# Kernel tuning notes

Measured on AMD Instinct MI355X. Metric: run time of the kernel, lower is better.

Reference implementation:

```python
import jax, jax.numpy as jnp
import numpy as np

B, L = 8192, 16
H, DK, DV = 8, 32, 32
DM, BN, V = 256, 128, 50000
NEG = -1e32  # mask_fill_value from masked_softmax(memory_efficient=True)


def layer_norm(x, g, b, eps=1e-5):
    m = jnp.mean(x, axis=-1, keepdims=True)
    var = jnp.mean((x - m) ** 2, axis=-1, keepdims=True)
    return (x - m) / jnp.sqrt(var + eps) * g + b


def setup_inputs() -> dict:
    key = jax.random.key(0)
    ks = iter(jax.random.split(key, 40))

    def n(shape, s):
        return jax.random.normal(next(ks), shape, jnp.float32) * s

    s_qk = float(np.sqrt(2.0 / (DM + DK)))
    s_v = float(np.sqrt(2.0 / (DM + DV)))
    d = {"x": jax.random.randint(next(ks), (B, L), 0, V)}
    d.update({
        "node_emb": n((V, BN), 1.0),
        "ln1_g": jnp.ones(BN), "ln1_b": jnp.zeros(BN),
        "ln2_g": jnp.ones(BN), "ln2_b": jnp.zeros(BN),
        "ln3_g": jnp.ones(BN), "ln3_b": jnp.zeros(BN),
        "Wq": n((H * DK, BN), s_qk), "Wk": n((H * DK, BN), s_qk), "Wv": n((H * DV, BN), s_v),
        "Wfc1": n((DM, H * DV), 0.05),
        "p1_w1": n((DM, DM), 0.05), "p1_b1": jnp.zeros(DM),
        "p1_w2": n((DM, DM), 0.05), "p1_b2": jnp.zeros(DM),
        "p1_lng": jnp.ones(DM), "p1_lnb": jnp.zeros(DM),
        "p2_w1": n((DM, BN), 0.05), "p2_b1": jnp.zeros(DM),
        "p2_w2": n((DM, DM), 0.05), "p2_b2": jnp.zeros(DM),
        "lnc1_g": jnp.ones(DM), "lnc1_b": jnp.zeros(DM),
        "lnc2_g": jnp.ones(DM), "lnc2_b": jnp.zeros(DM),
        "Wcls": n((1, DM), 0.05), "bcls": jnp.zeros(1),
    })
    return d


def reference(x, node_emb, ln1_g, ln1_b, ln2_g, ln2_b, ln3_g, ln3_b,
              Wq, Wk, Wv, Wfc1,
              p1_w1, p1_b1, p1_w2, p1_b2, p1_lng, p1_lnb,
              p2_w1, p2_b1, p2_w2, p2_b2,
              lnc1_g, lnc1_b, lnc2_g, lnc2_b, Wcls, bcls):
    b, l = x.shape
    emb = node_emb[x]                                  # [B,L,BN]
    npm = (x != 0).astype(jnp.float32)[..., None]      # non-pad mask [B,L,1]
    # MultiHeadAttention (eval mode, dropout off). Note: the slf_attn_mask
    # positional arg is overwritten inside forward by the ones-minus-eye
    # diag mask, and mask=None, so only diagonal self-exclusion applies.
    q = (layer_norm(emb, ln1_g, ln1_b) @ Wq.T).reshape(b, l, H, DK)
    k = (layer_norm(emb, ln2_g, ln2_b) @ Wk.T).reshape(b, l, H, DK)
    v = (layer_norm(emb, ln3_g, ln3_b) @ Wv.T).reshape(b, l, H, DV)
    scores = jnp.einsum('blhd,bmhd->bhlm', q, k) / jnp.sqrt(jnp.float32(DK))
    scores = jnp.where(jnp.eye(l, dtype=bool), NEG, scores)
    attn = jax.nn.softmax(scores, axis=-1)
    ctx = jnp.einsum('bhlm,bmhd->blhd', attn, v).reshape(b, l, H * DV)
    # fc1 + pff_n1 (residual + layer_norm since dims equal)
    dyn_in = (ctx @ Wfc1.T) * npm
    h1 = jnp.tanh(dyn_in @ p1_w1.T + p1_b1)
    dynamic = layer_norm(h1 @ p1_w2.T + p1_b2 + dyn_in, p1_lng, p1_lnb) * npm
    # pff_n2 on original (static) embedding; bottle_neck != d_model so no
    # residual / layer_norm. (The MHA fc2 static output is discarded by
    # EncoderLayer, so it is not computed here.)
    sta_in = emb * npm
    static = (jnp.tanh(sta_in @ p2_w1.T + p2_b1) @ p2_w2.T + p2_b2) * npm
    # Classifier head: diag_mask_flag=='True' -> (dynamic - static)**2
    dyn = layer_norm(dynamic, lnc1_g, lnc1_b)
    sta = layer_norm(static, lnc2_g, lnc2_b)
    probs = jax.nn.sigmoid((dyn - sta) ** 2 @ Wcls.T + bcls)  # [B,L,1]
    return jnp.sum(probs * npm, axis=1) / jnp.sum(npm, axis=1)  # [B,1]
```

## Files before the change

kernel.cpp:

```cpp
#include <hip/hip_runtime.h>
#include <math.h>

typedef unsigned short u16;
typedef _Float16 f16;
typedef f16 f16x4 __attribute__((ext_vector_type(4)));
typedef f16 f16x8v __attribute__((ext_vector_type(8)));
typedef float f32x4 __attribute__((ext_vector_type(4)));


__device__ __forceinline__ float tanh_f(float x) {
  float e = __expf(2.f * x);
  return 1.f - 2.f / (e + 1.f);
}

__device__ __forceinline__ void stage_chunk(const u16* __restrict__ wall, u16* wbuf,
                                            int si, int ds, int wid, int lane) {
  const u16* src = wall + (size_t)si * 8192;
  u16* dst = wbuf + ds * 8192;
#pragma unroll
  for (int j = 0; j < 2; ++j) {
    __builtin_amdgcn_global_load_lds(
        (const __attribute__((address_space(1))) void*)(src + j * 4096 + wid * 512 + lane * 8),
        (__attribute__((address_space(3))) void*)(dst + j * 4096 + wid * 512), 16, 0, 0);
  }
}

__device__ __forceinline__ const u16* pipe_acq(const u16* __restrict__ wall, u16* wbuf,
                                               int c, int wid, int lane) {
  int nx = c + 2;
  if (nx >= 48) nx -= 48;
  stage_chunk(wall, wbuf, nx, (c + 2) & 3, wid, lane);
  asm volatile("s_waitcnt vmcnt(4)" ::: "memory");
  __builtin_amdgcn_sched_barrier(0);
  __builtin_amdgcn_s_barrier();
  __builtin_amdgcn_sched_barrier(0);
  return wbuf + (c & 3) * 8192;
}

template <int PT, bool SW>
__device__ __forceinline__ f32x4 tile_mm32(const u16* buf, int lt, const f16x8v* bfr,
                                           int lane) {
  f32x4 a = {};
#pragma unroll
  for (int p = 0; p < PT; ++p) {
    f16x8v w = *(const f16x8v*)(buf + (lt * PT + p) * 512 + (size_t)lane * 8);
    if constexpr (!SW)
      a = __builtin_amdgcn_mfma_f32_16x16x32_f16(w, bfr[p], a, 0, 0, 0);
    else
      a = __builtin_amdgcn_mfma_f32_16x16x32_f16(bfr[p], w, a, 0, 0, 0);
  }
  return a;
}

__global__ __launch_bounds__(512) void fused_kernel(
    const int* __restrict__ x, const float* __restrict__ node_emb,
    const u16* __restrict__ wall, const float* __restrict__ aux,
    const float* __restrict__ p1_b1, const float* __restrict__ p1_b2,
    const float* __restrict__ p1_lng, const float* __restrict__ p1_lnb,
    const float* __restrict__ p2_b1, const float* __restrict__ p2_b2,
    const float* __restrict__ lnc1_g, const float* __restrict__ lnc1_b,
    const float* __restrict__ lnc2_g, const float* __restrict__ lnc2_b,
    const float* __restrict__ Wcls, const float* __restrict__ bcls,
    float* __restrict__ out) {
  __shared__ __align__(16) u16 wbuf[32768];
  const int lane = threadIdx.x & 63;
  const int wid = threadIdx.x >> 6;
  const int sr = lane & 15, g = lane >> 4;
  const int elem = blockIdx.x * 8 + wid;

  const int xi = x[elem * 16 + sr];
  const float npm = (xi != 0) ? 1.f : 0.f;

  stage_chunk(wall, wbuf, 0, 0, wid, lane);
  stage_chunk(wall, wbuf, 1, 1, wid, lane);

  f16x8v ebf8[4];
  float mu, rs;
  {
    const float4* erow = (const float4*)(node_emb + (size_t)xi * 128 + g * 4);
    float su = 0.f, sq = 0.f;
#pragma unroll
    for (int t = 0; t < 8; ++t) {
      float4 v = erow[t * 4];
      su += v.x + v.y + v.z + v.w;
      sq += v.x * v.x + v.y * v.y + v.z * v.z + v.w * v.w;
      const int hb = (t & 1) * 4;
      ebf8[t >> 1][hb + 0] = (f16)v.x;
      ebf8[t >> 1][hb + 1] = (f16)v.y;
      ebf8[t >> 1][hb + 2] = (f16)v.z;
      ebf8[t >> 1][hb + 3] = (f16)v.w;
    }
    su += __shfl_xor(su, 16); su += __shfl_xor(su, 32);
    sq += __shfl_xor(sq, 16); sq += __shfl_xor(sq, 32);
    mu = su * (1.f / 128.f);
    rs = rsqrtf(sq * (1.f / 128.f) - mu * mu + 1e-5f);
  }

  int c = 0;

  f16x8v qf8[8];
#pragma unroll
  for (int cc = 0; cc < 4; ++cc) {
    const u16* buf = pipe_acq(wall, wbuf, c, wid, lane);
#pragma unroll
    for (int lt = 0; lt < 4; ++lt) {
      f32x4 a = tile_mm32<4, false>(buf, lt, ebf8, lane);
      const int T = cc * 4 + lt;
      float4 G4 = *(const float4*)(aux + T * 16 + g * 4);
      float4 B4 = *(const float4*)(aux + 256 + T * 16 + g * 4);
      const int hb = (T & 1) * 4;
#pragma unroll
      for (int i = 0; i < 4; ++i)
        qf8[T >> 1][hb + i] =
            (f16)(rs * (a[i] - mu * ((const float*)&G4)[i]) + ((const float*)&B4)[i]);
    }
    ++c;
  }

  f16x4 pb[8];
#pragma unroll
  for (int cc = 0; cc < 4; ++cc) {
    const u16* buf = pipe_acq(wall, wbuf, c, wid, lane);
#pragma unroll
    for (int hh = 0; hh < 2; ++hh) {
      f16x8v kt8;
#pragma unroll
      for (int sub = 0; sub < 2; ++sub) {
        f32x4 a = tile_mm32<4, false>(buf, hh * 2 + sub, ebf8, lane);
        const int T = cc * 4 + hh * 2 + sub;
        float4 G4 = *(const float4*)(aux + 512 + T * 16 + g * 4);
        float4 B4 = *(const float4*)(aux + 512 + 256 + T * 16 + g * 4);
#pragma unroll
        for (int i = 0; i < 4; ++i)
          kt8[sub * 4 + i] =
              (f16)(rs * (a[i] - mu * ((const float*)&G4)[i]) + ((const float*)&B4)[i]);
      }
      const int h = cc * 2 + hh;
      f32x4 s4 = {};
      s4 = __builtin_amdgcn_mfma_f32_16x16x32_f16(kt8, qf8[h], s4, 0, 0, 0);
      float e4[4], mx = -3.0e38f;
#pragma unroll
      for (int i = 0; i < 4; ++i) {
        float v = s4[i] * 0.17677669529663687f;
        if ((g * 4 + i) == sr) v = -3.0e38f;
        e4[i] = v;
        mx = fmaxf(mx, v);
      }
      mx = fmaxf(mx, __shfl_xor(mx, 16));
      mx = fmaxf(mx, __shfl_xor(mx, 32));
      float sm = 0.f;
#pragma unroll
      for (int i = 0; i < 4; ++i) {
        e4[i] = ((g * 4 + i) == sr) ? 0.f : __expf(e4[i] - mx);
        sm += e4[i];
      }
      sm += __shfl_xor(sm, 16);
      sm += __shfl_xor(sm, 32);
      float inv = 1.f / sm;
#pragma unroll
      for (int i = 0; i < 4; ++i) pb[h][i] = (f16)(e4[i] * inv);
    }
    ++c;
  }

  f16x8v cf8[8];
  {
    float mur[4], rsr[4];
#pragma unroll
    for (int i = 0; i < 4; ++i) {
      mur[i] = __shfl(mu, g * 4 + i);
      rsr[i] = __shfl(rs, g * 4 + i);
    }
#pragma unroll
    for (int cc = 0; cc < 4; ++cc) {
      const u16* buf = pipe_acq(wall, wbuf, c, wid, lane);
#pragma unroll
      for (int lt = 0; lt < 4; ++lt) {
        f32x4 a = tile_mm32<4, true>(buf, lt, ebf8, lane);
        const int T = cc * 4 + lt;
        float Gv = aux[1024 + T * 16 + sr];
        float Bv = aux[1024 + 256 + T * 16 + sr];
        f16x4 vt;
#pragma unroll
        for (int i = 0; i < 4; ++i) vt[i] = (f16)(rsr[i] * (a[i] - mur[i] * Gv) + Bv);
        f32x4 cacc = {};
        cacc = __builtin_amdgcn_mfma_f32_16x16x16f16(vt, pb[T >> 1], cacc, 0, 0, 0);
        const int hb = (T & 1) * 4;
#pragma unroll
        for (int i = 0; i < 4; ++i) cf8[T >> 1][hb + i] = (f16)cacc[i];
      }
      ++c;
    }
  }

  f16x8v dinf8[8];
#pragma unroll
  for (int cc = 0; cc < 8; ++cc) {
    const u16* buf = pipe_acq(wall, wbuf, c, wid, lane);
#pragma unroll
    for (int lt = 0; lt < 2; ++lt) {
      f32x4 a = tile_mm32<8, false>(buf, lt, cf8, lane);
      const int T = cc * 2 + lt;
      const int hb = (T & 1) * 4;
#pragma unroll
      for (int i = 0; i < 4; ++i) dinf8[T >> 1][hb + i] = (f16)(a[i] * npm);
    }
    ++c;
  }

  f16x8v h1f8[8];
#pragma unroll
  for (int cc = 0; cc < 8; ++cc) {
    const u16* buf = pipe_acq(wall, wbuf, c, wid, lane);
#pragma unroll
    for (int lt = 0; lt < 2; ++lt) {
      f32x4 a = tile_mm32<8, false>(buf, lt, dinf8, lane);
      const int T = cc * 2 + lt;
      float4 b = *(const float4*)(p1_b1 + T * 16 + g * 4);
      const int hb = (T & 1) * 4;
#pragma unroll
      for (int i = 0; i < 4; ++i)
        h1f8[T >> 1][hb + i] = (f16)tanh_f(a[i] + ((const float*)&b)[i]);
    }
    ++c;
  }

  f16x4 d1f[16];
  float s1 = 0.f, s2 = 0.f;
#pragma unroll
  for (int cc = 0; cc < 8; ++cc) {
    const u16* buf = pipe_acq(wall, wbuf, c, wid, lane);
#pragma unroll
    for (int lt = 0; lt < 2; ++lt) {
      f32x4 a = tile_mm32<8, false>(buf, lt, h1f8, lane);
      const int T = cc * 2 + lt;
      float4 b = *(const float4*)(p1_b2 + T * 16 + g * 4);
      const int hb = (T & 1) * 4;
#pragma unroll
      for (int i = 0; i < 4; ++i) {
        float v = a[i] + ((const float*)&b)[i] + (float)dinf8[T >> 1][hb + i];
        s1 += v;
        s2 += v * v;
        d1f[T][i] = (f16)v;
      }
    }
    ++c;
  }
  s1 += __shfl_xor(s1, 16); s1 += __shfl_xor(s1, 32);
  s2 += __shfl_xor(s2, 16); s2 += __shfl_xor(s2, 32);
  const float muA = s1 * (1.f / 256.f);
  const float rsA = rsqrtf(s2 * (1.f / 256.f) - muA * muA + 1e-5f);

  f16x8v s1f8[8];
#pragma unroll
  for (int cc = 0; cc < 4; ++cc) {
    const u16* buf = pipe_acq(wall, wbuf, c, wid, lane);
#pragma unroll
    for (int lt = 0; lt < 4; ++lt) {
      f32x4 a = tile_mm32<4, false>(buf, lt, ebf8, lane);
      const int T = cc * 4 + lt;
      float4 b = *(const float4*)(p2_b1 + T * 16 + g * 4);
      const int hb = (T & 1) * 4;
#pragma unroll
      for (int i = 0; i < 4; ++i)
        s1f8[T >> 1][hb + i] = (f16)tanh_f(npm * a[i] + ((const float*)&b)[i]);
    }
    ++c;
  }

  float M_puu = 0.f, M_qvv = 0.f, M_pquv = 0.f;
  float M_pug = 0.f, M_ppu = 0.f, M_pqu = 0.f;
  float M_qvg = 0.f, M_pqv = 0.f, M_qqv = 0.f;
  float t1 = 0.f, t2 = 0.f, v1 = 0.f, v2 = 0.f;
#pragma unroll
  for (int cc = 0; cc < 8; ++cc) {
    const u16* buf = pipe_acq(wall, wbuf, c, wid, lane);
#pragma unroll
    for (int lt = 0; lt < 2; ++lt) {
      f32x4 av = tile_mm32<8, false>(buf, lt, s1f8, lane);
      const int T = cc * 2 + lt;
      float4 b2 = *(const float4*)(p2_b2 + T * 16 + g * 4);
      float4 lg = *(const float4*)(p1_lng + T * 16 + g * 4);
      float4 lb = *(const float4*)(p1_lnb + T * 16 + g * 4);
      float4 wc = *(const float4*)(Wcls + T * 16 + g * 4);
      float4 pg4 = *(const float4*)(lnc1_g + T * 16 + g * 4);
      float4 qg4 = *(const float4*)(lnc2_g + T * 16 + g * 4);
      float4 eb4 = *(const float4*)(lnc1_b + T * 16 + g * 4);
      float4 fb4 = *(const float4*)(lnc2_b + T * 16 + g * 4);
#pragma unroll
      for (int i = 0; i < 4; ++i) {
        float v = (av[i] + ((const float*)&b2)[i]) * npm;
        float u = (((float)d1f[T][i] - muA) * rsA * ((const float*)&lg)[i] +
                   ((const float*)&lb)[i]) * npm;
        t1 += u; t2 += u * u; v1 += v; v2 += v * v;
        float gc = ((const float*)&eb4)[i] - ((const float*)&fb4)[i];
        float pu = ((const float*)&pg4)[i] * u;
        float qv = ((const float*)&qg4)[i] * v;
        float wpu = ((const float*)&wc)[i] * pu;
        float wqv = ((const float*)&wc)[i] * qv;
        M_puu = fmaf(wpu, pu, M_puu);
        M_qvv = fmaf(wqv, qv, M_qvv);
        M_pquv = fmaf(wpu, qv, M_pquv);
        M_pug = fmaf(wpu, gc, M_pug);
        M_ppu = fmaf(wpu, ((const float*)&pg4)[i], M_ppu);
        M_pqu = fmaf(wpu, ((const float*)&qg4)[i], M_pqu);
        M_qvg = fmaf(wqv, gc, M_qvg);
        M_pqv = fmaf(wqv, ((const float*)&pg4)[i], M_pqv);
        M_qqv = fmaf(wqv, ((const float*)&qg4)[i], M_qqv);
      }
    }
    ++c;
  }
  asm volatile("s_waitcnt vmcnt(0)" ::: "memory");

#define RED2(z) z += __shfl_xor(z, 16); z += __shfl_xor(z, 32);
  RED2(t1) RED2(t2) RED2(v1) RED2(v2)
  RED2(M_puu) RED2(M_qvv) RED2(M_pquv)
  RED2(M_pug) RED2(M_ppu) RED2(M_pqu)
  RED2(M_qvg) RED2(M_pqv) RED2(M_qqv)
#undef RED2
  const float muD = t1 * (1.f / 256.f);
  const float aD = rsqrtf(t2 * (1.f / 256.f) - muD * muD + 1e-5f);
  const float muS = v1 * (1.f / 256.f);
  const float bS = rsqrtf(v2 * (1.f / 256.f) - muS * muS + 1e-5f);
  const float* s6 = aux + 1536;
  float logit = aD * aD * M_puu + bS * bS * M_qvv - 2.f * aD * bS * M_pquv
      + 2.f * aD * (M_pug - aD * muD * M_ppu + bS * muS * M_pqu)
      - 2.f * bS * (M_qvg - aD * muD * M_pqv + bS * muS * M_qqv)
      + s6[0] - 2.f * aD * muD * s6[1] + 2.f * bS * muS * s6[2]
      + aD * aD * muD * muD * s6[3] + bS * bS * muS * muS * s6[4]
      - 2.f * aD * bS * muD * muS * s6[5]
      + bcls[0];
  float prob = npm / (1.f + __expf(-logit));
  float ns = npm;
#pragma unroll
  for (int o = 1; o < 16; o <<= 1) {
    prob += __shfl_xor(prob, o);
    ns += __shfl_xor(ns, o);
  }
  if (lane == 0) out[elem] = prob / ns;
}

__global__ void prep_all(const float* __restrict__ Wq, const float* __restrict__ Wk,
                         const float* __restrict__ Wv, const float* __restrict__ Wfc1,
                         const float* __restrict__ p1w1, const float* __restrict__ p1w2,
                         const float* __restrict__ p2w1, const float* __restrict__ p2w2,
                         const float* __restrict__ g1, const float* __restrict__ b1,
                         const float* __restrict__ g2, const float* __restrict__ b2,
                         const float* __restrict__ g3, const float* __restrict__ b3,
                         const float* __restrict__ c1g, const float* __restrict__ c1b,
                         const float* __restrict__ c2g, const float* __restrict__ c2b,
                         const float* __restrict__ Wc,
                         u16* __restrict__ ws, float* __restrict__ aux) {
  int bx = blockIdx.x, t = threadIdx.x;
  if (bx == 1539) {
    if (t == 0) {
      float mgg = 0.f, mpg = 0.f, mqg = 0.f, mpp = 0.f, mqq = 0.f, mpq = 0.f;
      for (int cx = 0; cx < 256; ++cx) {
        float W = Wc[cx], p = c1g[cx], q = c2g[cx], gg = c1b[cx] - c2b[cx];
        mgg += W * gg * gg; mpg += W * p * gg; mqg += W * q * gg;
        mpp += W * p * p; mqq += W * q * q; mpq += W * p * q;
      }
      aux[1536] = mgg; aux[1537] = mpg; aux[1538] = mqg;
      aux[1539] = mpp; aux[1540] = mqq; aux[1541] = mpq;
    }
    return;
  }
  if (bx >= 1536) {
    int m = bx - 1536;
    const float* W = (m == 0) ? Wq : (m == 1) ? Wk : Wv;
    const float* gg = (m == 0) ? g1 : (m == 1) ? g2 : g3;
    const float* bb = (m == 0) ? b1 : (m == 1) ? b2 : b3;
    float G = 0.f, Bv = 0.f;
    for (int k = 0; k < 128; ++k) {
      float w = W[t * 128 + k];
      G += w * gg[k];
      Bv += w * bb[k];
    }
    aux[m * 512 + t] = G;
    aux[m * 512 + 256 + t] = Bv;
    return;
  }
  const float* src;
  u16* dst;
  const float* sc = nullptr;
  int base, K;
  if (bx < 128) {
    src = Wq; dst = ws; sc = g1; base = bx; K = 128;
  } else if (bx < 256) {
    src = Wk; dst = ws + 32768; sc = g2; base = bx - 128; K = 128;
  } else if (bx < 384) {
    src = Wv; dst = ws + 65536; sc = g3; base = bx - 256; K = 128;
  } else if (bx < 640) {
    src = Wfc1; dst = ws + 98304; base = bx - 384; K = 256;
  } else if (bx < 896) {
    src = p1w1; dst = ws + 163840; base = bx - 640; K = 256;
  } else if (bx < 1152) {
    src = p1w2; dst = ws + 229376; base = bx - 896; K = 256;
  } else if (bx < 1280) {
    src = p2w1; dst = ws + 294912; base = bx - 1152; K = 128;
  } else {
    src = p2w2; dst = ws + 327680; base = bx - 1280; K = 256;
  }
  int i = base * 256 + t;
  int n, k;
  if (K == 128) {
    n = i >> 7; k = i & 127;
  } else {
    n = i >> 8; k = i & 255;
  }
  float v = src[i];
  if (sc) v *= sc[k];
  int blk = (n >> 4) * (K >> 4) + (k >> 4);
  int l = (((k >> 2) & 3) << 4) + (n & 15);
  int di = ((blk >> 1) << 9) + (l << 3) + ((blk & 1) << 2) + (k & 3);
  dst[di] = __builtin_bit_cast(u16, (f16)v);
}

extern "C" void kernel_launch(void* const* d_in, const int* in_sizes, int n_in,
                              void* d_out, int out_size, void* d_ws, size_t ws_size,
                              hipStream_t stream) {
  const int* x = (const int*)d_in[0];
  const float* node_emb = (const float*)d_in[1];
  const float* ln1_g = (const float*)d_in[2];
  const float* ln1_b = (const float*)d_in[3];
  const float* ln2_g = (const float*)d_in[4];
  const float* ln2_b = (const float*)d_in[5];
  const float* ln3_g = (const float*)d_in[6];
  const float* ln3_b = (const float*)d_in[7];
  const float* Wq = (const float*)d_in[8];
  const float* Wk = (const float*)d_in[9];
  const float* Wv = (const float*)d_in[10];
  const float* Wfc1 = (const float*)d_in[11];
  const float* p1_w1 = (const float*)d_in[12];
  const float* p1_b1 = (const float*)d_in[13];
  const float* p1_w2 = (const float*)d_in[14];
  const float* p1_b2 = (const float*)d_in[15];
  const float* p1_lng = (const float*)d_in[16];
  const float* p1_lnb = (const float*)d_in[17];
  const float* p2_w1 = (const float*)d_in[18];
  const float* p2_b1 = (const float*)d_in[19];
  const float* p2_w2 = (const float*)d_in[20];
  const float* p2_b2 = (const float*)d_in[21];
  const float* lnc1_g = (const float*)d_in[22];
  const float* lnc1_b = (const float*)d_in[23];
  const float* lnc2_g = (const float*)d_in[24];
  const float* lnc2_b = (const float*)d_in[25];
  const float* Wcls = (const float*)d_in[26];
  const float* bcls = (const float*)d_in[27];

  u16* ws = (u16*)d_ws;
  float* aux = (float*)(ws + 393216);

  prep_all<<<1540, 256, 0, stream>>>(Wq, Wk, Wv, Wfc1, p1_w1, p1_w2, p2_w1, p2_w2, ln1_g, ln1_b,
                                     ln2_g, ln2_b, ln3_g, ln3_b, lnc1_g, lnc1_b, lnc2_g, lnc2_b,
                                     Wcls, ws, aux);

  const int B = in_sizes[0] / 16;
  fused_kernel<<<B / 8, 512, 0, stream>>>(
      x, node_emb, ws, aux, p1_b1, p1_b2, p1_lng, p1_lnb, p2_b1, p2_b2, lnc1_g, lnc1_b, lnc2_g,
      lnc2_b, Wcls, bcls, (float*)d_out);
}
```

Before: 212.9 us.

## Shrink blocks to 4 waves with smaller chunks and 3-deep 5-buffer weight pipeline

Each block now has 256 threads covering 4 batch elements instead of 512 threads and 8, so twice as many blocks are launched. Weight chunks are halved to 8 KB, staged three ahead into a 5-slot LDS ring (40 KB rather than 64 KB), and every stage loop is re-tiled so it consumes 96 chunks instead of 48. The aim is lower LDS use per block, more resident blocks and deeper prefetch that hides global-to-LDS latency. In exchange there are twice as many block barriers per element and each loaded weight chunk is reused by only 4 waves, which raises weight traffic.

```diff
diff --git a/kernel.cpp b/kernel.cpp
--- a/kernel.cpp
+++ b/kernel.cpp
@@ -15,26 +15,27 @@
 
 __device__ __forceinline__ void stage_chunk(const u16* __restrict__ wall, u16* wbuf,
                                             int si, int ds, int wid, int lane) {
-  const u16* src = wall + (size_t)si * 8192;
-  u16* dst = wbuf + ds * 8192;
+  const u16* src = wall + (size_t)si * 4096;
+  u16* dst = wbuf + ds * 4096;
 #pragma unroll
   for (int j = 0; j < 2; ++j) {
+    int seg = wid * 2 + j;
     __builtin_amdgcn_global_load_lds(
-        (const __attribute__((address_space(1))) void*)(src + j * 4096 + wid * 512 + lane * 8),
-        (__attribute__((address_space(3))) void*)(dst + j * 4096 + wid * 512), 16, 0, 0);
+        (const __attribute__((address_space(1))) void*)(src + seg * 512 + lane * 8),
+        (__attribute__((address_space(3))) void*)(dst + seg * 512), 16, 0, 0);
   }
 }
 
 __device__ __forceinline__ const u16* pipe_acq(const u16* __restrict__ wall, u16* wbuf,
                                                int c, int wid, int lane) {
-  int nx = c + 2;
-  if (nx >= 48) nx -= 48;
-  stage_chunk(wall, wbuf, nx, (c + 2) & 3, wid, lane);
-  asm volatile("s_waitcnt vmcnt(4)" ::: "memory");
+  int nx = c + 3;
+  if (nx >= 96) nx -= 96;
+  stage_chunk(wall, wbuf, nx, (c + 3) % 5, wid, lane);
+  asm volatile("s_waitcnt vmcnt(6)" ::: "memory");
   __builtin_amdgcn_sched_barrier(0);
   __builtin_amdgcn_s_barrier();
   __builtin_amdgcn_sched_barrier(0);
-  return wbuf + (c & 3) * 8192;
+  return wbuf + (c % 5) * 4096;
 }
 
 template <int PT, bool SW>
@@ -52,7 +53,7 @@
   return a;
 }
 
-__global__ __launch_bounds__(512) void fused_kernel(
+__global__ __launch_bounds__(256) void fused_kernel(
     const int* __restrict__ x, const float* __restrict__ node_emb,
     const u16* __restrict__ wall, const float* __restrict__ aux,
     const float* __restrict__ p1_b1, const float* __restrict__ p1_b2,
@@ -62,17 +63,18 @@
     const float* __restrict__ lnc2_g, const float* __restrict__ lnc2_b,
     const float* __restrict__ Wcls, const float* __restrict__ bcls,
     float* __restrict__ out) {
-  __shared__ __align__(16) u16 wbuf[32768];
+  __shared__ __align__(16) u16 wbuf[20480];
   const int lane = threadIdx.x & 63;
   const int wid = threadIdx.x >> 6;
   const int sr = lane & 15, g = lane >> 4;
-  const int elem = blockIdx.x * 8 + wid;
+  const int elem = blockIdx.x * 4 + wid;
 
   const int xi = x[elem * 16 + sr];
   const float npm = (xi != 0) ? 1.f : 0.f;
 
   stage_chunk(wall, wbuf, 0, 0, wid, lane);
   stage_chunk(wall, wbuf, 1, 1, wid, lane);
+  stage_chunk(wall, wbuf, 2, 2, wid, lane);
 
   f16x8v ebf8[4];
   float mu, rs;
@@ -100,12 +102,12 @@
 
   f16x8v qf8[8];
 #pragma unroll
-  for (int cc = 0; cc < 4; ++cc) {
-    const u16* buf = pipe_acq(wall, wbuf, c, wid, lane);
-#pragma unroll
-    for (int lt = 0; lt < 4; ++lt) {
+  for (int cc = 0; cc < 8; ++cc) {
+    const u16* buf = pipe_acq(wall, wbuf, c, wid, lane);
+#pragma unroll
+    for (int lt = 0; lt < 2; ++lt) {
       f32x4 a = tile_mm32<4, false>(buf, lt, ebf8, lane);
-      const int T = cc * 4 + lt;
+      const int T = cc * 2 + lt;
       float4 G4 = *(const float4*)(aux + T * 16 + g * 4);
       float4 B4 = *(const float4*)(aux + 256 + T * 16 + g * 4);
       const int hb = (T & 1) * 4;
@@ -119,47 +121,43 @@
 
   f16x4 pb[8];
 #pragma unroll
-  for (int cc = 0; cc < 4; ++cc) {
-    const u16* buf = pipe_acq(wall, wbuf, c, wid, lane);
-#pragma unroll
-    for (int hh = 0; hh < 2; ++hh) {
-      f16x8v kt8;
-#pragma unroll
-      for (int sub = 0; sub < 2; ++sub) {
-        f32x4 a = tile_mm32<4, false>(buf, hh * 2 + sub, ebf8, lane);
-        const int T = cc * 4 + hh * 2 + sub;
-        float4 G4 = *(const float4*)(aux + 512 + T * 16 + g * 4);
-        float4 B4 = *(const float4*)(aux + 512 + 256 + T * 16 + g * 4);
-#pragma unroll
-        for (int i = 0; i < 4; ++i)
-          kt8[sub * 4 + i] =
-              (f16)(rs * (a[i] - mu * ((const float*)&G4)[i]) + ((const float*)&B4)[i]);
-      }
-      const int h = cc * 2 + hh;
-      f32x4 s4 = {};
-      s4 = __builtin_amdgcn_mfma_f32_16x16x32_f16(kt8, qf8[h], s4, 0, 0, 0);
-      float e4[4], mx = -3.0e38f;
-#pragma unroll
-      for (int i = 0; i < 4; ++i) {
-        float v = s4[i] * 0.17677669529663687f;
-        if ((g * 4 + i) == sr) v = -3.0e38f;
-        e4[i] = v;
-        mx = fmaxf(mx, v);
-      }
-      mx = fmaxf(mx, __shfl_xor(mx, 16));
-      mx = fmaxf(mx, __shfl_xor(mx, 32));
-      float sm = 0.f;
-#pragma unroll
-      for (int i = 0; i < 4; ++i) {
-        e4[i] = ((g * 4 + i) == sr) ? 0.f : __expf(e4[i] - mx);
-        sm += e4[i];
-      }
-      sm += __shfl_xor(sm, 16);
-      sm += __shfl_xor(sm, 32);
-      float inv = 1.f / sm;
-#pragma unroll
-      for (int i = 0; i < 4; ++i) pb[h][i] = (f16)(e4[i] * inv);
-    }
+  for (int cc = 0; cc < 8; ++cc) {
+    const u16* buf = pipe_acq(wall, wbuf, c, wid, lane);
+    f16x8v kt8;
+#pragma unroll
+    for (int sub = 0; sub < 2; ++sub) {
+      f32x4 a = tile_mm32<4, false>(buf, sub, ebf8, lane);
+      const int T = cc * 2 + sub;
+      float4 G4 = *(const float4*)(aux + 512 + T * 16 + g * 4);
+      float4 B4 = *(const float4*)(aux + 512 + 256 + T * 16 + g * 4);
+#pragma unroll
+      for (int i = 0; i < 4; ++i)
+        kt8[sub * 4 + i] =
+            (f16)(rs * (a[i] - mu * ((const float*)&G4)[i]) + ((const float*)&B4)[i]);
+    }
+    f32x4 s4 = {};
+    s4 = __builtin_amdgcn_mfma_f32_16x16x32_f16(kt8, qf8[cc], s4, 0, 0, 0);
+    float e4[4], mx = -3.0e38f;
+#pragma unroll
+    for (int i = 0; i < 4; ++i) {
+      float v = s4[i] * 0.17677669529663687f;
+      if ((g * 4 + i) == sr) v = -3.0e38f;
+      e4[i] = v;
+      mx = fmaxf(mx, v);
+    }
+    mx = fmaxf(mx, __shfl_xor(mx, 16));
+    mx = fmaxf(mx, __shfl_xor(mx, 32));
+    float sm = 0.f;
+#pragma unroll
+    for (int i = 0; i < 4; ++i) {
+      e4[i] = ((g * 4 + i) == sr) ? 0.f : __expf(e4[i] - mx);
+      sm += e4[i];
+    }
+    sm += __shfl_xor(sm, 16);
+    sm += __shfl_xor(sm, 32);
+    float inv = 1.f / sm;
+#pragma unroll
+    for (int i = 0; i < 4; ++i) pb[cc][i] = (f16)(e4[i] * inv);
     ++c;
   }
 
@@ -172,12 +170,12 @@
       rsr[i] = __shfl(rs, g * 4 + i);
     }
 #pragma unroll
-    for (int cc = 0; cc < 4; ++cc) {
+    for (int cc = 0; cc < 8; ++cc) {
       const u16* buf = pipe_acq(wall, wbuf, c, wid, lane);
 #pragma unroll
-      for (int lt = 0; lt < 4; ++lt) {
+      for (int lt = 0; lt < 2; ++lt) {
         f32x4 a = tile_mm32<4, true>(buf, lt, ebf8, lane);
-        const int T = cc * 4 + lt;
+        const int T = cc * 2 + lt;
         float Gv = aux[1024 + T * 16 + sr];
         float Bv = aux[1024 + 256 + T * 16 + sr];
         f16x4 vt;
@@ -195,54 +193,42 @@
 
   f16x8v dinf8[8];
 #pragma unroll
-  for (int cc = 0; cc < 8; ++cc) {
-    const u16* buf = pipe_acq(wall, wbuf, c, wid, lane);
-#pragma unroll
-    for (int lt = 0; lt < 2; ++lt) {
-      f32x4 a = tile_mm32<8, false>(buf, lt, cf8, lane);
-      const int T = cc * 2 + lt;
-      const int hb = (T & 1) * 4;
-#pragma unroll
-      for (int i = 0; i < 4; ++i) dinf8[T >> 1][hb + i] = (f16)(a[i] * npm);
-    }
+  for (int T = 0; T < 16; ++T) {
+    const u16* buf = pipe_acq(wall, wbuf, c, wid, lane);
+    f32x4 a = tile_mm32<8, false>(buf, 0, cf8, lane);
+    const int hb = (T & 1) * 4;
+#pragma unroll
+    for (int i = 0; i < 4; ++i) dinf8[T >> 1][hb + i] = (f16)(a[i] * npm);
     ++c;
   }
 
   f16x8v h1f8[8];
 #pragma unroll
-  for (int cc = 0; cc < 8; ++cc) {
-    const u16* buf = pipe_acq(wall, wbuf, c, wid, lane);
-#pragma unroll
-    for (int lt = 0; lt < 2; ++lt) {
-      f32x4 a = tile_mm32<8, false>(buf, lt, dinf8, lane);
-      const int T = cc * 2 + lt;
-      float4 b = *(const float4*)(p1_b1 + T * 16 + g * 4);
-      const int hb = (T & 1) * 4;
-#pragma unroll
-      for (int i = 0; i < 4; ++i)
-        h1f8[T >> 1][hb + i] = (f16)tanh_f(a[i] + ((const float*)&b)[i]);
-    }
+  for (int T = 0; T < 16; ++T) {
+    const u16* buf = pipe_acq(wall, wbuf, c, wid, lane);
+    f32x4 a = tile_mm32<8, false>(buf, 0, dinf8, lane);
+    float4 b = *(const float4*)(p1_b1 + T * 16 + g * 4);
+    const int hb = (T & 1) * 4;
+#pragma unroll
+    for (int i = 0; i < 4; ++i)
+      h1f8[T >> 1][hb + i] = (f16)tanh_f(a[i] + ((const float*)&b)[i]);
     ++c;
   }
 
   f16x4 d1f[16];
   float s1 = 0.f, s2 = 0.f;
 #pragma unroll
-  for (int cc = 0; cc < 8; ++cc) {
-    const u16* buf = pipe_acq(wall, wbuf, c, wid, lane);
-#pragma unroll
-    for (int lt = 0; lt < 2; ++lt) {
-      f32x4 a = tile_mm32<8, false>(buf, lt, h1f8, lane);
-      const int T = cc * 2 + lt;
-      float4 b = *(const float4*)(p1_b2 + T * 16 + g * 4);
-      const int hb = (T & 1) * 4;
-#pragma unroll
-      for (int i = 0; i < 4; ++i) {
-        float v = a[i] + ((const float*)&b)[i] + (float)dinf8[T >> 1][hb + i];
-        s1 += v;
-        s2 += v * v;
-        d1f[T][i] = (f16)v;
-      }
+  for (int T = 0; T < 16; ++T) {
+    const u16* buf = pipe_acq(wall, wbuf, c, wid, lane);
+    f32x4 a = tile_mm32<8, false>(buf, 0, h1f8, lane);
+    float4 b = *(const float4*)(p1_b2 + T * 16 + g * 4);
+    const int hb = (T & 1) * 4;
+#pragma unroll
+    for (int i = 0; i < 4; ++i) {
+      float v = a[i] + ((const float*)&b)[i] + (float)dinf8[T >> 1][hb + i];
+      s1 += v;
+      s2 += v * v;
+      d1f[T][i] = (f16)v;
     }
     ++c;
   }
@@ -253,12 +239,12 @@
 
   f16x8v s1f8[8];
 #pragma unroll
-  for (int cc = 0; cc < 4; ++cc) {
-    const u16* buf = pipe_acq(wall, wbuf, c, wid, lane);
-#pragma unroll
-    for (int lt = 0; lt < 4; ++lt) {
+  for (int cc = 0; cc < 8; ++cc) {
+    const u16* buf = pipe_acq(wall, wbuf, c, wid, lane);
+#pragma unroll
+    for (int lt = 0; lt < 2; ++lt) {
       f32x4 a = tile_mm32<4, false>(buf, lt, ebf8, lane);
-      const int T = cc * 4 + lt;
+      const int T = cc * 2 + lt;
       float4 b = *(const float4*)(p2_b1 + T * 16 + g * 4);
       const int hb = (T & 1) * 4;
 #pragma unroll
@@ -273,41 +259,37 @@
   float M_qvg = 0.f, M_pqv = 0.f, M_qqv = 0.f;
   float t1 = 0.f, t2 = 0.f, v1 = 0.f, v2 = 0.f;
 #pragma unroll
-  for (int cc = 0; cc < 8; ++cc) {
-    const u16* buf = pipe_acq(wall, wbuf, c, wid, lane);
-#pragma unroll
-    for (int lt = 0; lt < 2; ++lt) {
-      f32x4 av = tile_mm32<8, false>(buf, lt, s1f8, lane);
-      const int T = cc * 2 + lt;
-      float4 b2 = *(const float4*)(p2_b2 + T * 16 + g * 4);
-      float4 lg = *(const float4*)(p1_lng + T * 16 + g * 4);
-      float4 lb = *(const float4*)(p1_lnb + T * 16 + g * 4);
-      float4 wc = *(const float4*)(Wcls + T * 16 + g * 4);
-      float4 pg4 = *(const float4*)(lnc1_g + T * 16 + g * 4);
-      float4 qg4 = *(const float4*)(lnc2_g + T * 16 + g * 4);
-      float4 eb4 = *(const float4*)(lnc1_b + T * 16 + g * 4);
-      float4 fb4 = *(const float4*)(lnc2_b + T * 16 + g * 4);
-#pragma unroll
-      for (int i = 0; i < 4; ++i) {
-        float v = (av[i] + ((const float*)&b2)[i]) * npm;
-        float u = (((float)d1f[T][i] - muA) * rsA * ((const float*)&lg)[i] +
-                   ((const float*)&lb)[i]) * npm;
-        t1 += u; t2 += u * u; v1 += v; v2 += v * v;
-        float gc = ((const float*)&eb4)[i] - ((const float*)&fb4)[i];
-        float pu = ((const float*)&pg4)[i] * u;
-        float qv = ((const float*)&qg4)[i] * v;
-        float wpu = ((const float*)&wc)[i] * pu;
-        float wqv = ((const float*)&wc)[i] * qv;
-        M_puu = fmaf(wpu, pu, M_puu);
-        M_qvv = fmaf(wqv, qv, M_qvv);
-        M_pquv = fmaf(wpu, qv, M_pquv);
-        M_pug = fmaf(wpu, gc, M_pug);
-        M_ppu = fmaf(wpu, ((const float*)&pg4)[i], M_ppu);
-        M_pqu = fmaf(wpu, ((const float*)&qg4)[i], M_pqu);
-        M_qvg = fmaf(wqv, gc, M_qvg);
-        M_pqv = fmaf(wqv, ((const float*)&pg4)[i], M_pqv);
-        M_qqv = fmaf(wqv, ((const float*)&qg4)[i], M_qqv);
-      }
+  for (int T = 0; T < 16; ++T) {
+    const u16* buf = pipe_acq(wall, wbuf, c, wid, lane);
+    f32x4 av = tile_mm32<8, false>(buf, 0, s1f8, lane);
+    float4 b2 = *(const float4*)(p2_b2 + T * 16 + g * 4);
+    float4 lg = *(const float4*)(p1_lng + T * 16 + g * 4);
+    float4 lb = *(const float4*)(p1_lnb + T * 16 + g * 4);
+    float4 wc = *(const float4*)(Wcls + T * 16 + g * 4);
+    float4 pg4 = *(const float4*)(lnc1_g + T * 16 + g * 4);
+    float4 qg4 = *(const float4*)(lnc2_g + T * 16 + g * 4);
+    float4 eb4 = *(const float4*)(lnc1_b + T * 16 + g * 4);
+    float4 fb4 = *(const float4*)(lnc2_b + T * 16 + g * 4);
+#pragma unroll
+    for (int i = 0; i < 4; ++i) {
+      float v = (av[i] + ((const float*)&b2)[i]) * npm;
+      float u = (((float)d1f[T][i] - muA) * rsA * ((const float*)&lg)[i] +
+                 ((const float*)&lb)[i]) * npm;
+      t1 += u; t2 += u * u; v1 += v; v2 += v * v;
+      float gc = ((const float*)&eb4)[i] - ((const float*)&fb4)[i];
+      float pu = ((const float*)&pg4)[i] * u;
+      float qv = ((const float*)&qg4)[i] * v;
+      float wpu = ((const float*)&wc)[i] * pu;
+      float wqv = ((const float*)&wc)[i] * qv;
+      M_puu = fmaf(wpu, pu, M_puu);
+      M_qvv = fmaf(wqv, qv, M_qvv);
+      M_pquv = fmaf(wpu, qv, M_pquv);
+      M_pug = fmaf(wpu, gc, M_pug);
+      M_ppu = fmaf(wpu, ((const float*)&pg4)[i], M_ppu);
+      M_pqu = fmaf(wpu, ((const float*)&qg4)[i], M_pqu);
+      M_qvg = fmaf(wqv, gc, M_qvg);
+      M_pqv = fmaf(wqv, ((const float*)&pg4)[i], M_pqv);
+      M_qqv = fmaf(wqv, ((const float*)&qg4)[i], M_qqv);
     }
     ++c;
   }
@@ -457,7 +439,7 @@
                                      Wcls, ws, aux);
 
   const int B = in_sizes[0] / 16;
-  fused_kernel<<<B / 8, 512, 0, stream>>>(
+  fused_kernel<<<B / 4, 256, 0, stream>>>(
       x, node_emb, ws, aux, p1_b1, p1_b2, p1_lng, p1_lnb, p2_b1, p2_b2, lnc1_g, lnc1_b, lnc2_g,
       lnc2_b, Wcls, bcls, (float*)d_out);
 }
```

Result: slower. 231.3 us (+8.6%).
